# Performance work log

Measured on AMD Instinct MI355X. Metric: run time of the kernel, lower is better.

## Reference

```python
import jax, jax.numpy as jnp
import numpy as np

ATT_SCALE = 1.0  # att_scale_factor


def setup_inputs() -> dict:
    key = jax.random.key(0)
    k1, k2, k3, k4, k5 = jax.random.split(key, 5)
    B, P, IMG_D, SEQ_D, H = 64, 576, 1024, 1024, 512
    seq_features = jax.random.normal(k1, (B, SEQ_D), dtype=jnp.float32)
    img_features = jax.random.normal(k2, (B, P, IMG_D), dtype=jnp.float32)
    # torch nn.Linear weights: [out_features, in_features], scaled to typical init magnitude
    W_seq = jax.random.normal(k3, (H, SEQ_D), dtype=jnp.float32) * (1.0 / np.sqrt(SEQ_D))
    W_img = jax.random.normal(k4, (H, IMG_D), dtype=jnp.float32) * (1.0 / np.sqrt(IMG_D))
    W_w = jax.random.normal(k5, (1, H), dtype=jnp.float32) * (1.0 / np.sqrt(H))
    return {"seq_features": seq_features, "img_features": img_features,
            "W_seq": W_seq, "W_img": W_img, "W_w": W_w}


def reference(seq_features, img_features, W_seq, W_img, W_w):
    # tanh(SeqTrans(seq)) broadcast over patch dim (avoids explicit .repeat)
    seq_h = jnp.tanh(jnp.einsum('bd,hd->bh', seq_features, W_seq))          # [B, H]
    img_h = jnp.tanh(jnp.einsum('bpd,hd->bph', img_features, W_img))        # [B, P, H]
    attend = seq_h[:, None, :] * img_h                                       # [B, P, H]
    # Dropout is Identity (att_dropout=None)
    scores = ATT_SCALE * jnp.einsum('bph,oh->bpo', attend, W_w)              # [B, P, 1]
    alpha = jax.nn.softmax(scores, axis=1)                                   # softmax over patches
    # weighted sum over patches; alpha broadcasts over channel dim (no .repeat needed)
    attended_img = jnp.sum(img_features * alpha, axis=1)                     # [B, IMG_D]
    return attended_img
```

## Files before the change

kernel.cpp:

```cpp
#include <hip/hip_runtime.h>
#include <hip/hip_bf16.h>

#define BB 64
#define PP 576
#define DD 1024
#define HH 512

typedef __attribute__((ext_vector_type(4))) float f32x4;
typedef __attribute__((ext_vector_type(8))) short bf16x8;

__device__ __forceinline__ unsigned short f2bf(float f) {
    union { float f; unsigned u; } v; v.f = f;
    unsigned r = v.u + 0x7FFF + ((v.u >> 16) & 1);
    return (unsigned short)(r >> 16);
}

__device__ __forceinline__ float fast_tanh(float x) {
    float e = __expf(2.f * x);
    return 1.f - 2.f / (e + 1.f);
}

__device__ __forceinline__ void gload16(const void* g, void* l) {
    __builtin_amdgcn_global_load_lds((const __attribute__((address_space(1))) unsigned int*)g,
                                     (__attribute__((address_space(3))) unsigned int*)l,
                                     16, 0, 0);
}

__global__ __launch_bounds__(256) void k_convert(const float* __restrict__ w,
                                                 unsigned short* __restrict__ o) {
    int i = (blockIdx.x * 256 + threadIdx.x) * 4;
    f32x4 v = *(const f32x4*)(w + i);
    ushort4 r;
    r.x = f2bf(v.x); r.y = f2bf(v.y); r.z = f2bf(v.z); r.w = f2bf(v.w);
    *(ushort4*)(o + i) = r;
}

__global__ __launch_bounds__(128) void k_seq(const float* __restrict__ seq,
                                             const float* __restrict__ W_seq,
                                             const float* __restrict__ W_w,
                                             float* __restrict__ g) {
    int b = blockIdx.x;
    int h = blockIdx.y * 128 + threadIdx.x;
    __shared__ float s_seq[DD];
    #pragma unroll
    for (int i = 0; i < 8; i++) s_seq[threadIdx.x + i * 128] = seq[b * DD + threadIdx.x + i * 128];
    __syncthreads();
    const float* wr = W_seq + (size_t)h * DD;
    float acc = 0.f;
    #pragma unroll 4
    for (int d = 0; d < DD; d += 4) {
        f32x4 w4 = *(const f32x4*)(wr + d);
        acc += w4.x * s_seq[d] + w4.y * s_seq[d + 1] + w4.z * s_seq[d + 2] + w4.w * s_seq[d + 3];
    }
    g[b * HH + h] = fast_tanh(acc) * W_w[h];
}

__global__ __launch_bounds__(256, 4) void k_scores(const float* __restrict__ img,
                                                   const unsigned short* __restrict__ Wb,
                                                   const float* __restrict__ g,
                                                   float* __restrict__ sp) {
    int b = blockIdx.y;
    int rt = blockIdx.x % 9;
    int ch = blockIdx.x / 9;
    int p0 = rt * 64;
    int h0 = ch * 256;
    int tid = threadIdx.x;
    int w = tid >> 6, lane = tid & 63;

    __shared__ unsigned short As[64 * 64];
    __shared__ unsigned short Bs[256 * 64];

    float gr[4];
    #pragma unroll
    for (int n = 0; n < 4; ++n) gr[n] = g[b * HH + h0 + w * 64 + n * 16 + (lane & 15)];

    f32x4 acc[4][4];
    #pragma unroll
    for (int m = 0; m < 4; m++)
        #pragma unroll
        for (int n = 0; n < 4; n++) acc[m][n] = (f32x4)0.f;

    int ar = tid >> 2;
    const float* asrc = img + ((size_t)(b * PP + p0 + ar)) * DD + (tid & 3) * 16;
    int cp = (tid & 3) * 2;
    int aw0 = ar * 64 + ((cp ^ (ar & 7)) * 8);
    int aw1 = ar * 64 + (((cp + 1) ^ (ar & 7)) * 8);

    int brow_l = lane >> 3;
    int bchunk = lane & 7;

    for (int kr = 0; kr < 16; ++kr) {
        int k0 = kr * 64;
        if (kr) __syncthreads();
        #pragma unroll
        for (int i = 0; i < 8; ++i) {
            int hr = (w * 8 + i) * 8 + brow_l;
            const unsigned short* src = Wb + (size_t)(h0 + hr) * DD + k0 + ((bchunk ^ (hr & 7)) * 8);
            gload16(src, &Bs[(w * 8 + i) * 512]);
        }
        f32x4 v0 = *(const f32x4*)(asrc + k0);
        f32x4 v1 = *(const f32x4*)(asrc + k0 + 4);
        f32x4 v2 = *(const f32x4*)(asrc + k0 + 8);
        f32x4 v3 = *(const f32x4*)(asrc + k0 + 12);
        bf16x8 pa, pb;
        pa[0] = (short)f2bf(v0.x); pa[1] = (short)f2bf(v0.y);
        pa[2] = (short)f2bf(v0.z); pa[3] = (short)f2bf(v0.w);
        pa[4] = (short)f2bf(v1.x); pa[5] = (short)f2bf(v1.y);
        pa[6] = (short)f2bf(v1.z); pa[7] = (short)f2bf(v1.w);
        pb[0] = (short)f2bf(v2.x); pb[1] = (short)f2bf(v2.y);
        pb[2] = (short)f2bf(v2.z); pb[3] = (short)f2bf(v2.w);
        pb[4] = (short)f2bf(v3.x); pb[5] = (short)f2bf(v3.y);
        pb[6] = (short)f2bf(v3.z); pb[7] = (short)f2bf(v3.w);
        *(bf16x8*)&As[aw0] = pa;
        *(bf16x8*)&As[aw1] = pb;
        __syncthreads();

        #pragma unroll
        for (int ks = 0; ks < 2; ++ks) {
            int cbase = ks * 4 + (lane >> 4);
            bf16x8 af[4], bfv[4];
            #pragma unroll
            for (int m = 0; m < 4; ++m) {
                int row = m * 16 + (lane & 15);
                af[m] = *(const bf16x8*)&As[row * 64 + ((cbase ^ (row & 7)) * 8)];
            }
            #pragma unroll
            for (int n = 0; n < 4; ++n) {
                int hr = w * 64 + n * 16 + (lane & 15);
                bfv[n] = *(const bf16x8*)&Bs[hr * 64 + ((cbase ^ (hr & 7)) * 8)];
            }
            #pragma unroll
            for (int m = 0; m < 4; ++m)
                #pragma unroll
                for (int n = 0; n < 4; ++n)
                    acc[m][n] = __builtin_amdgcn_mfma_f32_16x16x32_bf16(af[m], bfv[n], acc[m][n], 0, 0, 0);
        }
    }

    float part[4][4];
    #pragma unroll
    for (int m = 0; m < 4; m++)
        #pragma unroll
        for (int j = 0; j < 4; j++) part[m][j] = 0.f;
    #pragma unroll
    for (int m = 0; m < 4; ++m)
        #pragma unroll
        for (int n = 0; n < 4; ++n) {
            float gv = gr[n];
            f32x4 v = acc[m][n];
            #pragma unroll
            for (int j = 0; j < 4; ++j) part[m][j] += fast_tanh(v[j]) * gv;
        }
    #pragma unroll
    for (int mask = 1; mask < 16; mask <<= 1)
        #pragma unroll
        for (int m = 0; m < 4; ++m)
            #pragma unroll
            for (int j = 0; j < 4; ++j)
                part[m][j] += __shfl_xor(part[m][j], mask, 64);

    __syncthreads();
    float* red = (float*)As;
    if ((lane & 15) == 0) {
        int hi = lane >> 4;
        #pragma unroll
        for (int m = 0; m < 4; ++m)
            #pragma unroll
            for (int j = 0; j < 4; ++j)
                red[w * 64 + m * 16 + hi * 4 + j] = part[m][j];
    }
    __syncthreads();
    if (tid < 64) {
        float s = red[tid] + red[64 + tid] + red[128 + tid] + red[192 + tid];
        sp[(size_t)ch * (BB * PP) + b * PP + p0 + tid] = s;
    }
}

__global__ __launch_bounds__(576) void k_softmax(const float* __restrict__ sp,
                                                 float* __restrict__ alpha) {
    int b = blockIdx.x;
    int t = threadIdx.x;
    __shared__ float red[9];
    float s = sp[b * PP + t] + sp[BB * PP + b * PP + t];
    float m = s;
    #pragma unroll
    for (int off = 32; off; off >>= 1) m = fmaxf(m, __shfl_xor(m, off, 64));
    int w = t >> 6;
    if ((t & 63) == 0) red[w] = m;
    __syncthreads();
    float gm = red[0];
    #pragma unroll
    for (int i = 1; i < 9; i++) gm = fmaxf(gm, red[i]);
    float e = __expf(s - gm);
    float sum = e;
    #pragma unroll
    for (int off = 32; off; off >>= 1) sum += __shfl_xor(sum, off, 64);
    __syncthreads();
    if ((t & 63) == 0) red[w] = sum;
    __syncthreads();
    float gsum = 0.f;
    #pragma unroll
    for (int i = 0; i < 9; i++) gsum += red[i];
    alpha[b * PP + t] = e / gsum;
}

__global__ __launch_bounds__(256) void k_attend(const float* __restrict__ img,
                                                const float* __restrict__ alpha,
                                                float* __restrict__ part) {
    int b = blockIdx.y;
    int pc = blockIdx.x;
    int t = threadIdx.x;
    __shared__ float al[64];
    if (t < 64) al[t] = alpha[b * PP + pc * 64 + t];
    __syncthreads();
    int d = t * 4;
    f32x4 acc = (f32x4)0.f;
    const float* base = img + ((size_t)b * PP + (size_t)pc * 64) * DD + d;
    #pragma unroll 4
    for (int i = 0; i < 64; i++) {
        f32x4 v = *(const f32x4*)(base + (size_t)i * DD);
        acc += al[i] * v;
    }
    float* o = part + ((size_t)pc * BB + b) * DD + d;
    *(f32x4*)o = acc;
}

__global__ __launch_bounds__(256) void k_reduce(const float* __restrict__ part,
                                                float* __restrict__ out) {
    int i = blockIdx.x * 256 + threadIdx.x;
    float s = 0.f;
    #pragma unroll
    for (int pc = 0; pc < 9; pc++) s += part[pc * (BB * DD) + i];
    out[i] = s;
}

extern "C" void kernel_launch(void* const* d_in, const int* in_sizes, int n_in,
                              void* d_out, int out_size, void* d_ws, size_t ws_size,
                              hipStream_t stream) {
    const float* seq   = (const float*)d_in[0];
    const float* img   = (const float*)d_in[1];
    const float* W_seq = (const float*)d_in[2];
    const float* W_img = (const float*)d_in[3];
    const float* W_w   = (const float*)d_in[4];
    float* out = (float*)d_out;

    char* ws = (char*)d_ws;
    unsigned short* Wb = (unsigned short*)ws;
    float* g      = (float*)(ws + 1048576);
    float* sp     = (float*)(ws + 1048576 + 131072);
    float* alpha  = (float*)(ws + 1048576 + 131072 + 294912);
    float* part   = (float*)(ws + 1048576 + 131072 + 294912 + 147456);

    k_convert<<<512, 256, 0, stream>>>(W_img, Wb);
    k_seq<<<dim3(BB, 4), 128, 0, stream>>>(seq, W_seq, W_w, g);
    k_scores<<<dim3(18, BB), 256, 0, stream>>>(img, Wb, g, sp);
    k_softmax<<<BB, 576, 0, stream>>>(sp, alpha);
    k_attend<<<dim3(9, BB), 256, 0, stream>>>(img, alpha, part);
    k_reduce<<<256, 256, 0, stream>>>(part, out);
}
```

Measured before the change: 135.2 us.

## Enlarge scores GEMM tile to 128 patches with 8 waves and packed bf16 convert

The scores kernel now uses 512-thread blocks covering 128 patch rows by 256 hidden units, arranged as a 2x4 wave grid. Each W_img tile loaded into LDS is reused across twice as many patch rows, roughly halving weight traffic and the total block count. The last row tile is partial because 576 is not a multiple of 128, so source row indices are clamped and out-of-range rows are not stored. The fp32-to-bf16 conversion now uses the packed v_cvt_pk_bf16_f32 instruction instead of manual rounding. Trade-offs are about 11% wasted compute in the padded tile, fewer blocks to fill the GPU, and a dropped occupancy hint.

Result: slower. 157.1 us (+16.3%).

```diff
diff --git a/kernel.cpp b/kernel.cpp
--- a/kernel.cpp
+++ b/kernel.cpp
@@ -24,6 +24,15 @@
     __builtin_amdgcn_global_load_lds((const __attribute__((address_space(1))) unsigned int*)g,
                                      (__attribute__((address_space(3))) unsigned int*)l,
                                      16, 0, 0);
+}
+
+__device__ __forceinline__ bf16x8 cvt8(f32x4 a, f32x4 b) {
+    union { bf16x8 v; unsigned u[4]; } r;
+    asm("v_cvt_pk_bf16_f32 %0, %1, %2" : "=v"(r.u[0]) : "v"(a.x), "v"(a.y));
+    asm("v_cvt_pk_bf16_f32 %0, %1, %2" : "=v"(r.u[1]) : "v"(a.z), "v"(a.w));
+    asm("v_cvt_pk_bf16_f32 %0, %1, %2" : "=v"(r.u[2]) : "v"(b.x), "v"(b.y));
+    asm("v_cvt_pk_bf16_f32 %0, %1, %2" : "=v"(r.u[3]) : "v"(b.z), "v"(b.w));
+    return r.v;
 }
 
 __global__ __launch_bounds__(256) void k_convert(const float* __restrict__ w,
@@ -55,24 +64,27 @@
     g[b * HH + h] = fast_tanh(acc) * W_w[h];
 }
 
-__global__ __launch_bounds__(256, 4) void k_scores(const float* __restrict__ img,
-                                                   const unsigned short* __restrict__ Wb,
-                                                   const float* __restrict__ g,
-                                                   float* __restrict__ sp) {
+__global__ __launch_bounds__(512) void k_scores(const float* __restrict__ img,
+                                                const unsigned short* __restrict__ Wb,
+                                                const float* __restrict__ g,
+                                                float* __restrict__ sp) {
     int b = blockIdx.y;
-    int rt = blockIdx.x % 9;
-    int ch = blockIdx.x / 9;
-    int p0 = rt * 64;
+    int rt = blockIdx.x >> 1;
+    int ch = blockIdx.x & 1;
+    int p0 = rt * 128;
     int h0 = ch * 256;
     int tid = threadIdx.x;
     int w = tid >> 6, lane = tid & 63;
-
-    __shared__ unsigned short As[64 * 64];
+    int wr = w >> 2, wc = w & 3;
+    int r15 = lane & 15;
+    int kq = lane >> 4;
+
+    __shared__ unsigned short As[128 * 64];
     __shared__ unsigned short Bs[256 * 64];
 
     float gr[4];
     #pragma unroll
-    for (int n = 0; n < 4; ++n) gr[n] = g[b * HH + h0 + w * 64 + n * 16 + (lane & 15)];
+    for (int n = 0; n < 4; ++n) gr[n] = g[b * HH + h0 + wc * 64 + n * 16 + r15];
 
     f32x4 acc[4][4];
     #pragma unroll
@@ -80,9 +92,10 @@
         #pragma unroll
         for (int n = 0; n < 4; n++) acc[m][n] = (f32x4)0.f;
 
-    int ar = tid >> 2;
-    const float* asrc = img + ((size_t)(b * PP + p0 + ar)) * DD + (tid & 3) * 16;
-    int cp = (tid & 3) * 2;
+    int ar = tid >> 2, acn = tid & 3;
+    int prow = p0 + ar; if (prow > PP - 1) prow = PP - 1;
+    const float* asrc = img + ((size_t)(b * PP + prow)) * DD + acn * 16;
+    int cp = acn * 2;
     int aw0 = ar * 64 + ((cp ^ (ar & 7)) * 8);
     int aw1 = ar * 64 + (((cp + 1) ^ (ar & 7)) * 8);
 
@@ -93,41 +106,32 @@
         int k0 = kr * 64;
         if (kr) __syncthreads();
         #pragma unroll
-        for (int i = 0; i < 8; ++i) {
-            int hr = (w * 8 + i) * 8 + brow_l;
+        for (int i = 0; i < 4; ++i) {
+            int hr = w * 32 + i * 8 + brow_l;
             const unsigned short* src = Wb + (size_t)(h0 + hr) * DD + k0 + ((bchunk ^ (hr & 7)) * 8);
-            gload16(src, &Bs[(w * 8 + i) * 512]);
+            gload16(src, &Bs[(w * 32 + i * 8) * 64]);
         }
         f32x4 v0 = *(const f32x4*)(asrc + k0);
         f32x4 v1 = *(const f32x4*)(asrc + k0 + 4);
         f32x4 v2 = *(const f32x4*)(asrc + k0 + 8);
         f32x4 v3 = *(const f32x4*)(asrc + k0 + 12);
-        bf16x8 pa, pb;
-        pa[0] = (short)f2bf(v0.x); pa[1] = (short)f2bf(v0.y);
-        pa[2] = (short)f2bf(v0.z); pa[3] = (short)f2bf(v0.w);
-        pa[4] = (short)f2bf(v1.x); pa[5] = (short)f2bf(v1.y);
-        pa[6] = (short)f2bf(v1.z); pa[7] = (short)f2bf(v1.w);
-        pb[0] = (short)f2bf(v2.x); pb[1] = (short)f2bf(v2.y);
-        pb[2] = (short)f2bf(v2.z); pb[3] = (short)f2bf(v2.w);
-        pb[4] = (short)f2bf(v3.x); pb[5] = (short)f2bf(v3.y);
-        pb[6] = (short)f2bf(v3.z); pb[7] = (short)f2bf(v3.w);
-        *(bf16x8*)&As[aw0] = pa;
-        *(bf16x8*)&As[aw1] = pb;
+        *(bf16x8*)&As[aw0] = cvt8(v0, v1);
+        *(bf16x8*)&As[aw1] = cvt8(v2, v3);
         __syncthreads();
 
         #pragma unroll
         for (int ks = 0; ks < 2; ++ks) {
-            int cbase = ks * 4 + (lane >> 4);
+            int cbase = ks * 4 + kq;
             bf16x8 af[4], bfv[4];
             #pragma unroll
             for (int m = 0; m < 4; ++m) {
-                int row = m * 16 + (lane & 15);
-                af[m] = *(const bf16x8*)&As[row * 64 + ((cbase ^ (row & 7)) * 8)];
+                int row = wr * 64 + m * 16 + r15;
+                af[m] = *(const bf16x8*)&As[row * 64 + ((cbase ^ (r15 & 7)) * 8)];
             }
             #pragma unroll
             for (int n = 0; n < 4; ++n) {
-                int hr = w * 64 + n * 16 + (lane & 15);
-                bfv[n] = *(const bf16x8*)&Bs[hr * 64 + ((cbase ^ (hr & 7)) * 8)];
+                int hr = wc * 64 + n * 16 + r15;
+                bfv[n] = *(const bf16x8*)&Bs[hr * 64 + ((cbase ^ (r15 & 7)) * 8)];
             }
             #pragma unroll
             for (int m = 0; m < 4; ++m)
@@ -161,17 +165,19 @@
 
     __syncthreads();
     float* red = (float*)As;
-    if ((lane & 15) == 0) {
+    if (r15 == 0) {
         int hi = lane >> 4;
         #pragma unroll
         for (int m = 0; m < 4; ++m)
             #pragma unroll
             for (int j = 0; j < 4; ++j)
-                red[w * 64 + m * 16 + hi * 4 + j] = part[m][j];
-    }
-    __syncthreads();
-    if (tid < 64) {
-        float s = red[tid] + red[64 + tid] + red[128 + tid] + red[192 + tid];
+                red[(wr * 4 + wc) * 64 + m * 16 + hi * 4 + j] = part[m][j];
+    }
+    __syncthreads();
+    if (tid < 128 && p0 + tid < PP) {
+        int wrt = tid >> 6, r = tid & 63;
+        float s = red[(wrt * 4 + 0) * 64 + r] + red[(wrt * 4 + 1) * 64 + r]
+                + red[(wrt * 4 + 2) * 64 + r] + red[(wrt * 4 + 3) * 64 + r];
         sp[(size_t)ch * (BB * PP) + b * PP + p0 + tid] = s;
     }
 }
@@ -253,7 +259,7 @@
 
     k_convert<<<512, 256, 0, stream>>>(W_img, Wb);
     k_seq<<<dim3(BB, 4), 128, 0, stream>>>(seq, W_seq, W_w, g);
-    k_scores<<<dim3(18, BB), 256, 0, stream>>>(img, Wb, g, sp);
+    k_scores<<<dim3(10, BB), 512, 0, stream>>>(img, Wb, g, sp);
     k_softmax<<<BB, 576, 0, stream>>>(sp, alpha);
     k_attend<<<dim3(9, BB), 256, 0, stream>>>(img, alpha, part);
     k_reduce<<<256, 256, 0, stream>>>(part, out);
```
